# Kernel optimization log

Hardware: AMD Instinct MI355X
Metric: run time of the kernel (lower is better)

The kernel has to match this reference:

```python
import jax, jax.numpy as jnp
import numpy as np

TOP_K = 2


def setup_inputs() -> dict:
    key = jax.random.key(0)
    k1, k2, k3, k4 = jax.random.split(key, 4)
    B, S, H, I, E = 2, 1024, 2048, 1408, 8
    hidden_states = jax.random.normal(k1, (B, S, H), dtype=jnp.float32)
    gate_w = jax.random.normal(k2, (E, H), dtype=jnp.float32) * (1.0 / np.sqrt(H))
    # stacked expert weights: gate_up_proj [E, 2I, H], down_proj [E, H, I] (torch Linear [out,in])
    w1 = jax.random.normal(k3, (E, 2 * I, H), dtype=jnp.float32) * (1.0 / np.sqrt(H))
    w2 = jax.random.normal(k4, (E, H, I), dtype=jnp.float32) * (1.0 / np.sqrt(I))
    return {"hidden_states": hidden_states, "gate_w": gate_w, "w1": w1, "w2": w2}


def reference(hidden_states, gate_w, w1, w2):
    B, S, H = hidden_states.shape
    E = gate_w.shape[0]
    T = B * S
    x = hidden_states.reshape(T, H)

    # --- gating: softmax -> top-k -> renormalize ---
    logits = jnp.einsum('th,eh->te', x, gate_w)            # [T, E]
    probs = jax.nn.softmax(logits, axis=-1)
    topw, sel = jax.lax.top_k(probs, TOP_K)                # [T, K]
    topw = topw / jnp.sum(topw, axis=-1, keepdims=True)

    # combine weights: [T, E], zero for unselected experts (equivalent to
    # dispatch/permute + per-token routing-weight scale + unpermute + sum)
    combine = jnp.zeros((T, E), dtype=x.dtype).at[
        jnp.arange(T)[:, None], sel].add(topw)

    # --- grouped expert FFN (computed densely per expert) ---
    gate_up = jnp.einsum('th,eoh->eto', x, w1)             # [E, T, 2I]
    g, u = jnp.split(gate_up, 2, axis=-1)
    act = jax.nn.silu(g) * u                               # SiluAndMul, [E, T, I]
    expert_out = jnp.einsum('eti,ehi->eth', act, w2)       # [E, T, H]

    # --- combine ---
    out = jnp.einsum('eth,te->th', expert_out, combine)    # [T, H]
    return out.reshape(B, S, H)
```

## Files before the change

### kernel.cpp

```cpp
#include <hip/hip_runtime.h>
#include <hip/hip_bf16.h>
#include <math.h>

#define T_TOK 2048
#define H_DIM 2048
#define I_DIM 1408
#define E_NUM 8
#define I2    2816

typedef __attribute__((ext_vector_type(8))) short short8;
typedef __attribute__((ext_vector_type(4))) float floatx4;
typedef __attribute__((ext_vector_type(8))) unsigned short ushort8;
typedef unsigned short u16;

__device__ __forceinline__ u16 f2bf(float x) {
    unsigned u = __builtin_bit_cast(unsigned, x);
    return (u16)((u + 0x7FFFu + ((u >> 16) & 1u)) >> 16);
}

__device__ __forceinline__ floatx4 mfma16(short8 a, short8 b, floatx4 c) {
    return __builtin_amdgcn_mfma_f32_16x16x32_bf16(a, b, c, 0, 0, 0);
}

__device__ __forceinline__ void gload16(const u16* g, u16* l) {
    __builtin_amdgcn_global_load_lds(
        (const __attribute__((address_space(1))) unsigned int*)g,
        (__attribute__((address_space(3))) unsigned int*)l, 16, 0, 0);
}

__device__ __forceinline__ int swz(int r) { return (r & 3) ^ ((r >> 2) & 3); }

__global__ void moe_gating(const float* __restrict__ x, const float* __restrict__ gw,
                           float* __restrict__ wts, int* __restrict__ counts,
                           int* __restrict__ entries) {
    const int lane = threadIdx.x & 63;
    const int wv   = threadIdx.x >> 6;
    const int t    = blockIdx.x * 4 + wv;
    float acc[E_NUM];
#pragma unroll
    for (int e = 0; e < E_NUM; ++e) acc[e] = 0.f;
    const float4* xr = (const float4*)(x + (size_t)t * H_DIM);
#pragma unroll
    for (int j = 0; j < 8; ++j) {
        float4 xv = xr[lane + 64 * j];
#pragma unroll
        for (int e = 0; e < E_NUM; ++e) {
            float4 g = ((const float4*)(gw + (size_t)e * H_DIM))[lane + 64 * j];
            acc[e] += xv.x * g.x + xv.y * g.y + xv.z * g.z + xv.w * g.w;
        }
    }
#pragma unroll
    for (int off = 32; off > 0; off >>= 1)
#pragma unroll
        for (int e = 0; e < E_NUM; ++e) acc[e] += __shfl_xor(acc[e], off, 64);

    if (lane == 0) {
        int a = 0; float la = acc[0];
        for (int e = 1; e < E_NUM; ++e) if (acc[e] > la) { la = acc[e]; a = e; }
        int b = (a == 0) ? 1 : 0; float lb = acc[b];
        for (int e = 0; e < E_NUM; ++e)
            if (e != a && acc[e] > lb) { lb = acc[e]; b = e; }
        float wa = 1.f / (1.f + expf(lb - la));
        wts[t * 2 + 0] = wa;
        wts[t * 2 + 1] = 1.f - wa;
        int p0 = atomicAdd(&counts[a], 1); entries[a * T_TOK + p0] = t * 2;
        int p1 = atomicAdd(&counts[b], 1); entries[b * T_TOK + p1] = t * 2 + 1;
    }
}

__global__ __launch_bounds__(256)
void cvt_bf16(const float* __restrict__ src, u16* __restrict__ dst, int n8) {
    int i = blockIdx.x * 256 + threadIdx.x;
    if (i >= n8) return;
    const float4* s4 = (const float4*)src;
    float4 a = s4[2 * i], b = s4[2 * i + 1];
    ushort8 o;
    o[0] = f2bf(a.x); o[1] = f2bf(a.y); o[2] = f2bf(a.z); o[3] = f2bf(a.w);
    o[4] = f2bf(b.x); o[5] = f2bf(b.y); o[6] = f2bf(b.z); o[7] = f2bf(b.w);
    *(ushort8*)(dst + (size_t)i * 8) = o;
}

template <bool BPRE>
__global__ __launch_bounds__(256)
void moe_mfma1(const u16* __restrict__ xb, const void* __restrict__ w1v,
               const int* __restrict__ counts, const int* __restrict__ entries,
               u16* __restrict__ act) {
    const int e  = blockIdx.z;
    const int ne = counts[e];
    const int tm = blockIdx.y;
    if (tm * 128 >= ne) return;
    const int tn = blockIdx.x;

    __shared__ __align__(16) u16 As[128 * 32];
    __shared__ __align__(16) u16 Bg[64 * 32];
    __shared__ __align__(16) u16 Bu[64 * 32];
    __shared__ int rowv[128];

    const int tid = threadIdx.x;
    if (tid < 128) {
        int r = tm * 128 + tid;
        rowv[tid] = (r < ne) ? entries[(size_t)e * T_TOK + r] : -1;
    }
    __syncthreads();

    const u16* asrc[2]; u16* adst[2];
#pragma unroll
    for (int q = 0; q < 2; ++q) {
        int i = q * 256 + tid;
        int row = i >> 2, p = i & 3;
        int lc = p ^ swz(row);
        int v = rowv[row];
        int tok = (v < 0) ? 0 : (v >> 1);
        asrc[q] = xb + (size_t)tok * H_DIM + lc * 8;
        adst[q] = As + i * 8;
    }
    const int brow = tid >> 2, bp = tid & 3;
    const int blc  = bp ^ swz(brow);
    const u16*   w1b = (const u16*)w1v;
    const float* w1f = (const float*)w1v;
    const size_t grow = ((size_t)e * I2 + tn * 64 + brow) * H_DIM + blc * 8;
    const size_t urow = grow + (size_t)I_DIM * H_DIM;
    u16* bgdst = Bg + tid * 8;
    u16* budst = Bu + tid * 8;

    const int lane = tid & 63, wid = tid >> 6;
    const int wm = wid & 1, wn = wid >> 1;

    floatx4 accG[4][2], accU[4][2];
    const floatx4 z4 = {0.f, 0.f, 0.f, 0.f};
#pragma unroll
    for (int mi = 0; mi < 4; ++mi)
#pragma unroll
        for (int ni = 0; ni < 2; ++ni) { accG[mi][ni] = z4; accU[mi][ni] = z4; }

    int aoff[4], boff[2];
#pragma unroll
    for (int mi = 0; mi < 4; ++mi) {
        int m = wm * 64 + mi * 16 + (lane & 15);
        aoff[mi] = m * 32 + (((lane >> 4) ^ swz(m)) * 8);
    }
#pragma unroll
    for (int ni = 0; ni < 2; ++ni) {
        int n = wn * 32 + ni * 16 + (lane & 15);
        boff[ni] = n * 32 + (((lane >> 4) ^ swz(n)) * 8);
    }

    for (int k0 = 0; k0 < H_DIM; k0 += 32) {
        gload16(asrc[0] + k0, adst[0]);
        gload16(asrc[1] + k0, adst[1]);
        if (BPRE) {
            gload16(w1b + grow + k0, bgdst);
            gload16(w1b + urow + k0, budst);
        } else {
            const float* gs = w1f + grow + k0;
            const float* us = w1f + urow + k0;
            float4 g0 = *(const float4*)gs, g1 = *(const float4*)(gs + 4);
            float4 u0 = *(const float4*)us, u1 = *(const float4*)(us + 4);
            ushort8 gv, uv;
            gv[0] = f2bf(g0.x); gv[1] = f2bf(g0.y); gv[2] = f2bf(g0.z); gv[3] = f2bf(g0.w);
            gv[4] = f2bf(g1.x); gv[5] = f2bf(g1.y); gv[6] = f2bf(g1.z); gv[7] = f2bf(g1.w);
            uv[0] = f2bf(u0.x); uv[1] = f2bf(u0.y); uv[2] = f2bf(u0.z); uv[3] = f2bf(u0.w);
            uv[4] = f2bf(u1.x); uv[5] = f2bf(u1.y); uv[6] = f2bf(u1.z); uv[7] = f2bf(u1.w);
            *(ushort8*)bgdst = gv;
            *(ushort8*)budst = uv;
        }
        __syncthreads();
        short8 a[4], bg[2], bu[2];
#pragma unroll
        for (int mi = 0; mi < 4; ++mi) a[mi] = *(const short8*)(As + aoff[mi]);
#pragma unroll
        for (int ni = 0; ni < 2; ++ni) {
            bg[ni] = *(const short8*)(Bg + boff[ni]);
            bu[ni] = *(const short8*)(Bu + boff[ni]);
        }
#pragma unroll
        for (int mi = 0; mi < 4; ++mi)
#pragma unroll
            for (int ni = 0; ni < 2; ++ni) {
                accG[mi][ni] = mfma16(a[mi], bg[ni], accG[mi][ni]);
                accU[mi][ni] = mfma16(a[mi], bu[ni], accU[mi][ni]);
            }
        __syncthreads();
    }

    const int obase = tn * 64 + wn * 32;
#pragma unroll
    for (int mi = 0; mi < 4; ++mi)
#pragma unroll
        for (int ni = 0; ni < 2; ++ni)
#pragma unroll
            for (int r = 0; r < 4; ++r) {
                int row = wm * 64 + mi * 16 + (lane >> 4) * 4 + r;
                int v = rowv[row];
                if (v < 0) continue;
                float g = accG[mi][ni][r], u = accU[mi][ni][r];
                float s = g / (1.f + expf(-g)) * u;
                act[(size_t)v * I_DIM + obase + ni * 16 + (lane & 15)] = f2bf(s);
            }
}

template <bool BPRE>
__global__ __launch_bounds__(256)
void moe_mfma2(const u16* __restrict__ act, const void* __restrict__ w2v,
               const int* __restrict__ counts, const int* __restrict__ entries,
               const float* __restrict__ wts, float* __restrict__ out) {
    const int e  = blockIdx.z;
    const int ne = counts[e];
    const int tm = blockIdx.y;
    if (tm * 128 >= ne) return;
    const int tn = blockIdx.x;

    __shared__ __align__(16) u16 As[128 * 32];
    __shared__ __align__(16) u16 Bs[128 * 32];
    __shared__ int   rowv[128];
    __shared__ int   rowt[128];
    __shared__ float roww[128];

    const int tid = threadIdx.x;
    if (tid < 128) {
        int r = tm * 128 + tid;
        int v = (r < ne) ? entries[(size_t)e * T_TOK + r] : -1;
        rowv[tid] = v;
        rowt[tid] = (v < 0) ? 0 : (v >> 1);
        roww[tid] = (v < 0) ? 0.f : wts[v];
    }
    __syncthreads();

    const u16* asrc[2]; u16* adst[2];
    size_t bsrc[2]; u16* bdst[2];
    const u16*   w2b = (const u16*)w2v;
    const float* w2f = (const float*)w2v;
#pragma unroll
    for (int q = 0; q < 2; ++q) {
        int i = q * 256 + tid;
        int row = i >> 2, p = i & 3;
        int lc = p ^ swz(row);
        int v = rowv[row]; if (v < 0) v = 0;
        asrc[q] = act + (size_t)v * I_DIM + lc * 8;
        adst[q] = As + i * 8;
        bsrc[q] = ((size_t)e * H_DIM + tn * 128 + row) * I_DIM + lc * 8;
        bdst[q] = Bs + i * 8;
    }

    const int lane = tid & 63, wid = tid >> 6;
    const int wm = wid & 1, wn = wid >> 1;

    floatx4 acc[4][4];
    const floatx4 z4 = {0.f, 0.f, 0.f, 0.f};
#pragma unroll
    for (int mi = 0; mi < 4; ++mi)
#pragma unroll
        for (int ni = 0; ni < 4; ++ni) acc[mi][ni] = z4;

    int aoff[4], boff[4];
#pragma unroll
    for (int mi = 0; mi < 4; ++mi) {
        int m = wm * 64 + mi * 16 + (lane & 15);
        aoff[mi] = m * 32 + (((lane >> 4) ^ swz(m)) * 8);
    }
#pragma unroll
    for (int ni = 0; ni < 4; ++ni) {
        int n = wn * 64 + ni * 16 + (lane & 15);
        boff[ni] = n * 32 + (((lane >> 4) ^ swz(n)) * 8);
    }

    for (int k0 = 0; k0 < I_DIM; k0 += 32) {
        gload16(asrc[0] + k0, adst[0]);
        gload16(asrc[1] + k0, adst[1]);
        if (BPRE) {
            gload16(w2b + bsrc[0] + k0, bdst[0]);
            gload16(w2b + bsrc[1] + k0, bdst[1]);
        } else {
#pragma unroll
            for (int q = 0; q < 2; ++q) {
                const float* bs = w2f + bsrc[q] + k0;
                float4 b0 = *(const float4*)bs, b1 = *(const float4*)(bs + 4);
                ushort8 bv;
                bv[0] = f2bf(b0.x); bv[1] = f2bf(b0.y); bv[2] = f2bf(b0.z); bv[3] = f2bf(b0.w);
                bv[4] = f2bf(b1.x); bv[5] = f2bf(b1.y); bv[6] = f2bf(b1.z); bv[7] = f2bf(b1.w);
                *(ushort8*)bdst[q] = bv;
            }
        }
        __syncthreads();
        short8 a[4], b[4];
#pragma unroll
        for (int mi = 0; mi < 4; ++mi) a[mi] = *(const short8*)(As + aoff[mi]);
#pragma unroll
        for (int ni = 0; ni < 4; ++ni) b[ni] = *(const short8*)(Bs + boff[ni]);
#pragma unroll
        for (int mi = 0; mi < 4; ++mi)
#pragma unroll
            for (int ni = 0; ni < 4; ++ni)
                acc[mi][ni] = mfma16(a[mi], b[ni], acc[mi][ni]);
        __syncthreads();
    }

    const int hbase = tn * 128 + wn * 64;
#pragma unroll
    for (int mi = 0; mi < 4; ++mi)
#pragma unroll
        for (int ni = 0; ni < 4; ++ni)
#pragma unroll
            for (int r = 0; r < 4; ++r) {
                int row = wm * 64 + mi * 16 + (lane >> 4) * 4 + r;
                if (rowv[row] < 0) continue;
                atomicAdd(out + (size_t)rowt[row] * H_DIM + hbase + ni * 16 + (lane & 15),
                          roww[row] * acc[mi][ni][r]);
            }
}

extern "C" void kernel_launch(void* const* d_in, const int* in_sizes, int n_in,
                              void* d_out, int out_size, void* d_ws, size_t ws_size,
                              hipStream_t stream) {
    const float* x  = (const float*)d_in[0];
    const float* gw = (const float*)d_in[1];
    const float* w1 = (const float*)d_in[2];
    const float* w2 = (const float*)d_in[3];
    float* out = (float*)d_out;

    char* ws = (char*)d_ws;
    int*   counts  = (int*)ws;
    int*   entries = (int*)(ws + 256);
    float* wts     = (float*)(ws + 256 + 65536);
    u16* xb  = (u16*)(ws + 131072);
    u16* act = xb  + (size_t)T_TOK * H_DIM;
    u16* w1b = act + (size_t)2 * T_TOK * I_DIM;
    u16* w2b = w1b + (size_t)E_NUM * I2 * H_DIM;
    const size_t need = 131072 + 2ull * ((size_t)T_TOK * H_DIM + 2ull * T_TOK * I_DIM +
                                         (size_t)E_NUM * I2 * H_DIM +
                                         (size_t)E_NUM * H_DIM * I_DIM);
    const bool pre = (ws_size >= need);

    hipMemsetAsync(counts, 0, 256, stream);
    hipMemsetAsync(out, 0, (size_t)T_TOK * H_DIM * sizeof(float), stream);

    moe_gating<<<T_TOK / 4, 256, 0, stream>>>(x, gw, wts, counts, entries);
    cvt_bf16<<<(T_TOK * H_DIM / 8 + 255) / 256, 256, 0, stream>>>(x, xb, T_TOK * H_DIM / 8);

    if (pre) {
        cvt_bf16<<<(E_NUM * I2 * H_DIM / 8 + 255) / 256, 256, 0, stream>>>(w1, w1b, E_NUM * I2 * H_DIM / 8);
        cvt_bf16<<<(E_NUM * H_DIM * I_DIM / 8 + 255) / 256, 256, 0, stream>>>(w2, w2b, E_NUM * H_DIM * I_DIM / 8);
        moe_mfma1<true><<<dim3(I_DIM / 64, 16, E_NUM), 256, 0, stream>>>(xb, w1b, counts, entries, act);
        moe_mfma2<true><<<dim3(H_DIM / 128, 16, E_NUM), 256, 0, stream>>>(act, w2b, counts, entries, wts, out);
    } else {
        moe_mfma1<false><<<dim3(I_DIM / 64, 16, E_NUM), 256, 0, stream>>>(xb, w1, counts, entries, act);
        moe_mfma2<false><<<dim3(H_DIM / 128, 16, E_NUM), 256, 0, stream>>>(act, w2, counts, entries, wts, out);
    }
}
```

Before: 567.3 us.

## Double-buffer MoE GEMMs, convert weights in-loop, fuse x conversion into gating

Removes the separate bf16 conversion passes for the expert weights and for x: x is converted inside the gating kernel, and fp32 weights are loaded into registers and converted while staging into shared memory. Both GEMM kernels use double-buffered LDS, prefetching the next K slice before computing the current one, so only one barrier per step is needed. The grid is reordered so token tiles vary fastest, letting blocks that share a weight tile run together and reuse it from cache. The tradeoff is that fp32 weights are re-read once per token tile instead of bf16 once, and conversion work now sits in the GEMM inner loop.

```diff
diff --git a/kernel.cpp b/kernel.cpp
--- a/kernel.cpp
+++ b/kernel.cpp
@@ -10,29 +10,33 @@
 
 typedef __attribute__((ext_vector_type(8))) short short8;
 typedef __attribute__((ext_vector_type(4))) float floatx4;
-typedef __attribute__((ext_vector_type(8))) unsigned short ushort8;
+typedef __attribute__((ext_vector_type(8))) unsigned short bhalf8;
+typedef __attribute__((ext_vector_type(4))) unsigned short bhalf4;
 typedef unsigned short u16;
 
 __device__ __forceinline__ u16 f2bf(float x) {
     unsigned u = __builtin_bit_cast(unsigned, x);
     return (u16)((u + 0x7FFFu + ((u >> 16) & 1u)) >> 16);
 }
-
+__device__ __forceinline__ bhalf8 pack8(float4 a, float4 b) {
+    bhalf8 o;
+    o[0] = f2bf(a.x); o[1] = f2bf(a.y); o[2] = f2bf(a.z); o[3] = f2bf(a.w);
+    o[4] = f2bf(b.x); o[5] = f2bf(b.y); o[6] = f2bf(b.z); o[7] = f2bf(b.w);
+    return o;
+}
 __device__ __forceinline__ floatx4 mfma16(short8 a, short8 b, floatx4 c) {
     return __builtin_amdgcn_mfma_f32_16x16x32_bf16(a, b, c, 0, 0, 0);
 }
-
 __device__ __forceinline__ void gload16(const u16* g, u16* l) {
     __builtin_amdgcn_global_load_lds(
         (const __attribute__((address_space(1))) unsigned int*)g,
         (__attribute__((address_space(3))) unsigned int*)l, 16, 0, 0);
 }
-
 __device__ __forceinline__ int swz(int r) { return (r & 3) ^ ((r >> 2) & 3); }
 
 __global__ void moe_gating(const float* __restrict__ x, const float* __restrict__ gw,
                            float* __restrict__ wts, int* __restrict__ counts,
-                           int* __restrict__ entries) {
+                           int* __restrict__ entries, u16* __restrict__ xb) {
     const int lane = threadIdx.x & 63;
     const int wv   = threadIdx.x >> 6;
     const int t    = blockIdx.x * 4 + wv;
@@ -43,6 +47,9 @@
 #pragma unroll
     for (int j = 0; j < 8; ++j) {
         float4 xv = xr[lane + 64 * j];
+        bhalf4 xo;
+        xo[0] = f2bf(xv.x); xo[1] = f2bf(xv.y); xo[2] = f2bf(xv.z); xo[3] = f2bf(xv.w);
+        *(bhalf4*)(xb + (size_t)t * H_DIM + 4 * (lane + 64 * j)) = xo;
 #pragma unroll
         for (int e = 0; e < E_NUM; ++e) {
             float4 g = ((const float4*)(gw + (size_t)e * H_DIM))[lane + 64 * j];
@@ -69,31 +76,16 @@
 }
 
 __global__ __launch_bounds__(256)
-void cvt_bf16(const float* __restrict__ src, u16* __restrict__ dst, int n8) {
-    int i = blockIdx.x * 256 + threadIdx.x;
-    if (i >= n8) return;
-    const float4* s4 = (const float4*)src;
-    float4 a = s4[2 * i], b = s4[2 * i + 1];
-    ushort8 o;
-    o[0] = f2bf(a.x); o[1] = f2bf(a.y); o[2] = f2bf(a.z); o[3] = f2bf(a.w);
-    o[4] = f2bf(b.x); o[5] = f2bf(b.y); o[6] = f2bf(b.z); o[7] = f2bf(b.w);
-    *(ushort8*)(dst + (size_t)i * 8) = o;
-}
-
-template <bool BPRE>
-__global__ __launch_bounds__(256)
-void moe_mfma1(const u16* __restrict__ xb, const void* __restrict__ w1v,
+void moe_mfma1(const u16* __restrict__ xb, const float* __restrict__ w1,
                const int* __restrict__ counts, const int* __restrict__ entries,
                u16* __restrict__ act) {
-    const int e  = blockIdx.z;
+    const int e = blockIdx.z, tn = blockIdx.y, tm = blockIdx.x;
     const int ne = counts[e];
-    const int tm = blockIdx.y;
     if (tm * 128 >= ne) return;
-    const int tn = blockIdx.x;
-
-    __shared__ __align__(16) u16 As[128 * 32];
-    __shared__ __align__(16) u16 Bg[64 * 32];
-    __shared__ __align__(16) u16 Bu[64 * 32];
+
+    __shared__ __align__(16) u16 As[2][128 * 32];
+    __shared__ __align__(16) u16 Bg[2][64 * 32];
+    __shared__ __align__(16) u16 Bu[2][64 * 32];
     __shared__ int rowv[128];
 
     const int tid = threadIdx.x;
@@ -103,25 +95,20 @@
     }
     __syncthreads();
 
-    const u16* asrc[2]; u16* adst[2];
+    const u16* asrc[2]; int adsti[2];
 #pragma unroll
     for (int q = 0; q < 2; ++q) {
         int i = q * 256 + tid;
         int row = i >> 2, p = i & 3;
         int lc = p ^ swz(row);
-        int v = rowv[row];
-        int tok = (v < 0) ? 0 : (v >> 1);
+        int v = rowv[row]; int tok = (v < 0) ? 0 : (v >> 1);
         asrc[q] = xb + (size_t)tok * H_DIM + lc * 8;
-        adst[q] = As + i * 8;
+        adsti[q] = i * 8;
     }
     const int brow = tid >> 2, bp = tid & 3;
     const int blc  = bp ^ swz(brow);
-    const u16*   w1b = (const u16*)w1v;
-    const float* w1f = (const float*)w1v;
-    const size_t grow = ((size_t)e * I2 + tn * 64 + brow) * H_DIM + blc * 8;
-    const size_t urow = grow + (size_t)I_DIM * H_DIM;
-    u16* bgdst = Bg + tid * 8;
-    u16* budst = Bu + tid * 8;
+    const float* gptr = w1 + ((size_t)e * I2 + tn * 64 + brow) * H_DIM + blc * 8;
+    const float* uptr = gptr + (size_t)I_DIM * H_DIM;
 
     const int lane = tid & 63, wid = tid >> 6;
     const int wm = wid & 1, wn = wid >> 1;
@@ -145,33 +132,30 @@
         boff[ni] = n * 32 + (((lane >> 4) ^ swz(n)) * 8);
     }
 
-    for (int k0 = 0; k0 < H_DIM; k0 += 32) {
-        gload16(asrc[0] + k0, adst[0]);
-        gload16(asrc[1] + k0, adst[1]);
-        if (BPRE) {
-            gload16(w1b + grow + k0, bgdst);
-            gload16(w1b + urow + k0, budst);
-        } else {
-            const float* gs = w1f + grow + k0;
-            const float* us = w1f + urow + k0;
-            float4 g0 = *(const float4*)gs, g1 = *(const float4*)(gs + 4);
-            float4 u0 = *(const float4*)us, u1 = *(const float4*)(us + 4);
-            ushort8 gv, uv;
-            gv[0] = f2bf(g0.x); gv[1] = f2bf(g0.y); gv[2] = f2bf(g0.z); gv[3] = f2bf(g0.w);
-            gv[4] = f2bf(g1.x); gv[5] = f2bf(g1.y); gv[6] = f2bf(g1.z); gv[7] = f2bf(g1.w);
-            uv[0] = f2bf(u0.x); uv[1] = f2bf(u0.y); uv[2] = f2bf(u0.z); uv[3] = f2bf(u0.w);
-            uv[4] = f2bf(u1.x); uv[5] = f2bf(u1.y); uv[6] = f2bf(u1.z); uv[7] = f2bf(u1.w);
-            *(ushort8*)bgdst = gv;
-            *(ushort8*)budst = uv;
+    float4 g0 = *(const float4*)gptr, g1 = *(const float4*)(gptr + 4);
+    float4 u0 = *(const float4*)uptr, u1 = *(const float4*)(uptr + 4);
+    gload16(asrc[0], &As[0][adsti[0]]);
+    gload16(asrc[1], &As[0][adsti[1]]);
+
+    for (int it = 0; it < H_DIM / 32; ++it) {
+        const int cb = it & 1;
+        *(bhalf8*)&Bg[cb][tid * 8] = pack8(g0, g1);
+        *(bhalf8*)&Bu[cb][tid * 8] = pack8(u0, u1);
+        __syncthreads();
+        if (it + 1 < H_DIM / 32) {
+            const int kn = (it + 1) * 32;
+            g0 = *(const float4*)(gptr + kn); g1 = *(const float4*)(gptr + kn + 4);
+            u0 = *(const float4*)(uptr + kn); u1 = *(const float4*)(uptr + kn + 4);
+            gload16(asrc[0] + kn, &As[cb ^ 1][adsti[0]]);
+            gload16(asrc[1] + kn, &As[cb ^ 1][adsti[1]]);
         }
-        __syncthreads();
         short8 a[4], bg[2], bu[2];
 #pragma unroll
-        for (int mi = 0; mi < 4; ++mi) a[mi] = *(const short8*)(As + aoff[mi]);
+        for (int mi = 0; mi < 4; ++mi) a[mi] = *(const short8*)&As[cb][aoff[mi]];
 #pragma unroll
         for (int ni = 0; ni < 2; ++ni) {
-            bg[ni] = *(const short8*)(Bg + boff[ni]);
-            bu[ni] = *(const short8*)(Bu + boff[ni]);
+            bg[ni] = *(const short8*)&Bg[cb][boff[ni]];
+            bu[ni] = *(const short8*)&Bu[cb][boff[ni]];
         }
 #pragma unroll
         for (int mi = 0; mi < 4; ++mi)
@@ -180,7 +164,6 @@
                 accG[mi][ni] = mfma16(a[mi], bg[ni], accG[mi][ni]);
                 accU[mi][ni] = mfma16(a[mi], bu[ni], accU[mi][ni]);
             }
-        __syncthreads();
     }
 
     const int obase = tn * 64 + wn * 32;
@@ -199,19 +182,16 @@
             }
 }
 
-template <bool BPRE>
 __global__ __launch_bounds__(256)
-void moe_mfma2(const u16* __restrict__ act, const void* __restrict__ w2v,
+void moe_mfma2(const u16* __restrict__ act, const float* __restrict__ w2,
                const int* __restrict__ counts, const int* __restrict__ entries,
                const float* __restrict__ wts, float* __restrict__ out) {
-    const int e  = blockIdx.z;
+    const int e = blockIdx.z, tn = blockIdx.y, tm = blockIdx.x;
     const int ne = counts[e];
-    const int tm = blockIdx.y;
     if (tm * 128 >= ne) return;
-    const int tn = blockIdx.x;
-
-    __shared__ __align__(16) u16 As[128 * 32];
-    __shared__ __align__(16) u16 Bs[128 * 32];
+
+    __shared__ __align__(16) u16 As[2][128 * 32];
+    __shared__ __align__(16) u16 Bs[2][128 * 32];
     __shared__ int   rowv[128];
     __shared__ int   rowt[128];
     __shared__ float roww[128];
@@ -226,10 +206,8 @@
     }
     __syncthreads();
 
-    const u16* asrc[2]; u16* adst[2];
-    size_t bsrc[2]; u16* bdst[2];
-    const u16*   w2b = (const u16*)w2v;
-    const float* w2f = (const float*)w2v;
+    const u16* asrc[2]; int adsti[2];
+    const float* bptr[2]; int bdsti[2];
 #pragma unroll
     for (int q = 0; q < 2; ++q) {
         int i = q * 256 + tid;
@@ -237,9 +215,9 @@
         int lc = p ^ swz(row);
         int v = rowv[row]; if (v < 0) v = 0;
         asrc[q] = act + (size_t)v * I_DIM + lc * 8;
-        adst[q] = As + i * 8;
-        bsrc[q] = ((size_t)e * H_DIM + tn * 128 + row) * I_DIM + lc * 8;
-        bdst[q] = Bs + i * 8;
+        adsti[q] = i * 8;
+        bptr[q] = w2 + ((size_t)e * H_DIM + tn * 128 + row) * I_DIM + lc * 8;
+        bdsti[q] = i * 8;
     }
 
     const int lane = tid & 63, wid = tid >> 6;
@@ -264,35 +242,33 @@
         boff[ni] = n * 32 + (((lane >> 4) ^ swz(n)) * 8);
     }
 
-    for (int k0 = 0; k0 < I_DIM; k0 += 32) {
-        gload16(asrc[0] + k0, adst[0]);
-        gload16(asrc[1] + k0, adst[1]);
-        if (BPRE) {
-            gload16(w2b + bsrc[0] + k0, bdst[0]);
-            gload16(w2b + bsrc[1] + k0, bdst[1]);
-        } else {
-#pragma unroll
-            for (int q = 0; q < 2; ++q) {
-                const float* bs = w2f + bsrc[q] + k0;
-                float4 b0 = *(const float4*)bs, b1 = *(const float4*)(bs + 4);
-                ushort8 bv;
-                bv[0] = f2bf(b0.x); bv[1] = f2bf(b0.y); bv[2] = f2bf(b0.z); bv[3] = f2bf(b0.w);
-                bv[4] = f2bf(b1.x); bv[5] = f2bf(b1.y); bv[6] = f2bf(b1.z); bv[7] = f2bf(b1.w);
-                *(ushort8*)bdst[q] = bv;
-            }
+    float4 b00 = *(const float4*)bptr[0], b01 = *(const float4*)(bptr[0] + 4);
+    float4 b10 = *(const float4*)bptr[1], b11 = *(const float4*)(bptr[1] + 4);
+    gload16(asrc[0], &As[0][adsti[0]]);
+    gload16(asrc[1], &As[0][adsti[1]]);
+
+    for (int it = 0; it < I_DIM / 32; ++it) {
+        const int cb = it & 1;
+        *(bhalf8*)&Bs[cb][bdsti[0]] = pack8(b00, b01);
+        *(bhalf8*)&Bs[cb][bdsti[1]] = pack8(b10, b11);
+        __syncthreads();
+        if (it + 1 < I_DIM / 32) {
+            const int kn = (it + 1) * 32;
+            b00 = *(const float4*)(bptr[0] + kn); b01 = *(const float4*)(bptr[0] + kn + 4);
+            b10 = *(const float4*)(bptr[1] + kn); b11 = *(const float4*)(bptr[1] + kn + 4);
+            gload16(asrc[0] + kn, &As[cb ^ 1][adsti[0]]);
+            gload16(asrc[1] + kn, &As[cb ^ 1][adsti[1]]);
         }
-        __syncthreads();
         short8 a[4], b[4];
 #pragma unroll
-        for (int mi = 0; mi < 4; ++mi) a[mi] = *(const short8*)(As + aoff[mi]);
-#pragma unroll
-        for (int ni = 0; ni < 4; ++ni) b[ni] = *(const short8*)(Bs + boff[ni]);
+        for (int mi = 0; mi < 4; ++mi) a[mi] = *(const short8*)&As[cb][aoff[mi]];
+#pragma unroll
+        for (int ni = 0; ni < 4; ++ni) b[ni] = *(const short8*)&Bs[cb][boff[ni]];
 #pragma unroll
         for (int mi = 0; mi < 4; ++mi)
 #pragma unroll
             for (int ni = 0; ni < 4; ++ni)
                 acc[mi][ni] = mfma16(a[mi], b[ni], acc[mi][ni]);
-        __syncthreads();
     }
 
     const int hbase = tn * 128 + wn * 64;
@@ -323,27 +299,12 @@
     int*   entries = (int*)(ws + 256);
     float* wts     = (float*)(ws + 256 + 65536);
     u16* xb  = (u16*)(ws + 131072);
-    u16* act = xb  + (size_t)T_TOK * H_DIM;
-    u16* w1b = act + (size_t)2 * T_TOK * I_DIM;
-    u16* w2b = w1b + (size_t)E_NUM * I2 * H_DIM;
-    const size_t need = 131072 + 2ull * ((size_t)T_TOK * H_DIM + 2ull * T_TOK * I_DIM +
-                                         (size_t)E_NUM * I2 * H_DIM +
-                                         (size_t)E_NUM * H_DIM * I_DIM);
-    const bool pre = (ws_size >= need);
-
-    hipMemsetAsync(counts, 0, 256, stream);
-    hipMemsetAsync(out, 0, (size_t)T_TOK * H_DIM * sizeof(float), stream);
-
-    moe_gating<<<T_TOK / 4, 256, 0, stream>>>(x, gw, wts, counts, entries);
-    cvt_bf16<<<(T_TOK * H_DIM / 8 + 255) / 256, 256, 0, stream>>>(x, xb, T_TOK * H_DIM / 8);
-
-    if (pre) {
-        cvt_bf16<<<(E_NUM * I2 * H_DIM / 8 + 255) / 256, 256, 0, stream>>>(w1, w1b, E_NUM * I2 * H_DIM / 8);
-        cvt_bf16<<<(E_NUM * H_DIM * I_DIM / 8 + 255) / 256, 256, 0, stream>>>(w2, w2b, E_NUM * H_DIM * I_DIM / 8);
-        moe_mfma1<true><<<dim3(I_DIM / 64, 16, E_NUM), 256, 0, stream>>>(xb, w1b, counts, entries, act);
-        moe_mfma2<true><<<dim3(H_DIM / 128, 16, E_NUM), 256, 0, stream>>>(act, w2b, counts, entries, wts, out);
-    } else {
-        moe_mfma1<false><<<dim3(I_DIM / 64, 16, E_NUM), 256, 0, stream>>>(xb, w1, counts, entries, act);
-        moe_mfma2<false><<<dim3(H_DIM / 128, 16, E_NUM), 256, 0, stream>>>(act, w2, counts, entries, wts, out);
-    }
-}
+    u16* act = xb + (size_t)T_TOK * H_DIM;
+
+    (void)hipMemsetAsync(counts, 0, 256, stream);
+    (void)hipMemsetAsync(out, 0, (size_t)T_TOK * H_DIM * sizeof(float), stream);
+
+    moe_gating<<<T_TOK / 4, 256, 0, stream>>>(x, gw, wts, counts, entries, xb);
+    moe_mfma1<<<dim3(16, I_DIM / 64, E_NUM), 256, 0, stream>>>(xb, w1, counts, entries, act);
+    moe_mfma2<<<dim3(16, H_DIM / 128, E_NUM), 256, 0, stream>>>(act, w2, counts, entries, wts, out);
+}
```

Result: slower. 852.8 us (+50.3%).
